# Performance work log

Hardware: AMD Instinct MI355X
Metric: run time of the kernel (lower is better)

The kernel has to match this reference:

```python
import jax, jax.numpy as jnp
import numpy as np

B, P, C = 8, 20000, 64
NX, NY = 432, 496


def setup_inputs() -> dict:
    key = jax.random.key(0)
    k1, k2 = jax.random.split(key)
    pillar_features = jax.random.normal(k1, (B, P, C), dtype=jnp.float32)
    # unique flat cell index per batch so scatter is order-independent
    flat = jax.vmap(lambda k: jax.random.permutation(k, NX * NY)[:P])(
        jax.random.split(k2, B)
    )  # (B, P) int32, unique within each batch
    y = (flat // NX).astype(jnp.int64)
    x = (flat % NX).astype(jnp.int64)
    b = jnp.broadcast_to(jnp.arange(B, dtype=jnp.int64)[:, None], (B, P))
    z = jnp.zeros((B, P), dtype=jnp.int64)
    coords = jnp.stack([b, z, y, x], axis=-1)  # (B, P, 4)
    return {"pillar_features": pillar_features, "coords": coords, "nx": NX, "ny": NY}


def reference(pillar_features, coords, nx, ny):
    # pillar_features: (B, P, C), coords: (B, P, 4) = [batch_idx, z, y, x]
    Bb, Pp, Cc = pillar_features.shape
    idx = coords[:, :, 2] * nx + coords[:, :, 3]          # (B, P) flat y*nx + x
    canvas = jnp.zeros((Bb, ny * nx, Cc), dtype=pillar_features.dtype)
    canvas = canvas.at[jnp.arange(Bb)[:, None], idx].set(pillar_features)
    return canvas.transpose(0, 2, 1).reshape(Bb, Cc, ny, nx)  # (B, C, ny, nx)
```

## Files before the change

### kernel.cpp

```cpp
#include <hip/hip_runtime.h>


#define BB    8
#define PP    20000
#define CC    64
#define NXX   432
#define NYY   496
#define NCELL (NXX * NYY)
#define NCELL4 (NCELL / 4)

#define GBLK   64
#define GNWG   ((BB * NCELL4) / GBLK)
#define NXCD   8
#define CHUNK  (GNWG / NXCD)

typedef float f32x4 __attribute__((ext_vector_type(4)));
typedef unsigned short u16;
typedef u16 u16x4 __attribute__((ext_vector_type(4)));

__global__ void ppsc_scatter_map(const int* __restrict__ coords, u16* __restrict__ map16) {
    int t = blockIdx.x * blockDim.x + threadIdx.x;
    if (t >= BB * PP) return;
    int b = t / PP;
    int p = t - b * PP;
    const int4 c4 = ((const int4*)coords)[t];
    int y = c4.z, x = c4.w;
    if ((unsigned)y < (unsigned)NYY && (unsigned)x < (unsigned)NXX)
        map16[(size_t)b * NCELL + y * NXX + x] = (u16)p;
}

__global__ void __launch_bounds__(GBLK, 8) ppsc_gather_all(const float* __restrict__ pf,
                                                           const u16* __restrict__ map16,
                                                           const int* __restrict__ coords,
                                                           float* __restrict__ out) {
    int bid = blockIdx.x;
    int wg  = (bid % NXCD) * CHUNK + bid / NXCD;

    int t  = wg * GBLK + threadIdx.x;
    int i4 = t % NCELL4;
    int b  = t / NCELL4;

    u16x4 m = ((const u16x4*)(map16 + (size_t)b * NCELL))[i4];
    const int4* cb = ((const int4*)coords) + (size_t)b * PP;
    int cell0 = i4 * 4;

    bool v0 = (m.x < PP), v1 = (m.y < PP), v2 = (m.z < PP), v3 = (m.w < PP);
    if (v0) { int4 c = cb[m.x]; v0 = (c.z * NXX + c.w) == cell0;     }
    if (v1) { int4 c = cb[m.y]; v1 = (c.z * NXX + c.w) == cell0 + 1; }
    if (v2) { int4 c = cb[m.z]; v2 = (c.z * NXX + c.w) == cell0 + 2; }
    if (v3) { int4 c = cb[m.w]; v3 = (c.z * NXX + c.w) == cell0 + 3; }

    const float* base = pf + (size_t)b * PP * CC;
    const float* p0 = base + (size_t)m.x * CC;
    const float* p1 = base + (size_t)m.y * CC;
    const float* p2 = base + (size_t)m.z * CC;
    const float* p3 = base + (size_t)m.w * CC;

    float* ob = out + (size_t)b * CC * NCELL + (size_t)cell0;

#pragma unroll 4
    for (int cq = 0; cq < 16; ++cq) {
        f32x4 o0 = (f32x4)0.f, o1 = (f32x4)0.f, o2 = (f32x4)0.f, o3 = (f32x4)0.f;
        if (v0) { f32x4 f = *(const f32x4*)(p0 + cq * 4);
                  o0.x = f.x; o1.x = f.y; o2.x = f.z; o3.x = f.w; }
        if (v1) { f32x4 f = *(const f32x4*)(p1 + cq * 4);
                  o0.y = f.x; o1.y = f.y; o2.y = f.z; o3.y = f.w; }
        if (v2) { f32x4 f = *(const f32x4*)(p2 + cq * 4);
                  o0.z = f.x; o1.z = f.y; o2.z = f.z; o3.z = f.w; }
        if (v3) { f32x4 f = *(const f32x4*)(p3 + cq * 4);
                  o0.w = f.x; o1.w = f.y; o2.w = f.z; o3.w = f.w; }
        float* op = ob + (size_t)(cq * 4) * NCELL;
        __builtin_nontemporal_store(o0, (f32x4*)op);
        __builtin_nontemporal_store(o1, (f32x4*)(op + (size_t)NCELL));
        __builtin_nontemporal_store(o2, (f32x4*)(op + 2 * (size_t)NCELL));
        __builtin_nontemporal_store(o3, (f32x4*)(op + 3 * (size_t)NCELL));
    }
}

__global__ void ppsc_zero(float* __restrict__ out, int n4) {
    int t = blockIdx.x * blockDim.x + threadIdx.x;
    if (t < n4) ((float4*)out)[t] = make_float4(0.f, 0.f, 0.f, 0.f);
}

__global__ void ppsc_direct_scatter(const float* __restrict__ pf,
                                    const int* __restrict__ coords,
                                    float* __restrict__ out) {
    int t = blockIdx.x * blockDim.x + threadIdx.x;
    if (t >= BB * PP * CC) return;
    int c  = t % CC;
    int bp = t / CC;
    int b  = bp / PP;
    const int* cd = coords + (size_t)bp * 4;
    int y = cd[2], x = cd[3];
    if ((unsigned)y < (unsigned)NYY && (unsigned)x < (unsigned)NXX)
        out[((size_t)(b * CC + c)) * NCELL + (size_t)y * NXX + x] = pf[(size_t)bp * CC + c];
}

extern "C" void kernel_launch(void* const* d_in, const int* in_sizes, int n_in,
                              void* d_out, int out_size, void* d_ws, size_t ws_size,
                              hipStream_t stream) {
    const float* pf     = (const float*)d_in[0];
    const int*   coords = (const int*)d_in[1];
    float*       out    = (float*)d_out;

    const size_t map_bytes = (size_t)BB * NCELL * sizeof(u16);

    if (ws_size >= map_bytes) {
        u16* map16 = (u16*)d_ws;

        int npil = BB * PP;
        ppsc_scatter_map<<<(npil + 255) / 256, 256, 0, stream>>>(coords, map16);

        ppsc_gather_all<<<GNWG, GBLK, 0, stream>>>(pf, map16, coords, out);
    } else {
        int n4_out = out_size / 4;
        ppsc_zero<<<(n4_out + 255) / 256, 256, 0, stream>>>(out, n4_out);

        int nsc = BB * PP * CC;
        ppsc_direct_scatter<<<(nsc + 255) / 256, 256, 0, stream>>>(pf, coords, out);
    }
}
```

Measured before the change: 94.67 us.

## Process two cell groups per thread in gather and XCD-swizzle scatter map

The gather kernel now handles two 4-cell groups per thread (first and second half of the canvas), halving the grid and doubling the loads and stores in flight per thread. The block-to-XCD swizzle is generalized to handle non-divisible grid sizes and is also applied to the scatter-map kernel, which now launches 64-thread blocks. The aim is more memory-level parallelism per wave and better L2 locality per XCD, at the cost of higher register use and possibly lower occupancy.

Result: slower. 130.1 us (+37.4%).

```diff
diff --git a/kernel.cpp b/kernel.cpp
--- a/kernel.cpp
+++ b/kernel.cpp
@@ -8,21 +8,33 @@
 #define NYY   496
 #define NCELL (NXX * NYY)
 #define NCELL4 (NCELL / 4)
+#define HALF4 (NCELL4 / 2)
 
 #define GBLK   64
-#define GNWG   ((BB * NCELL4) / GBLK)
+#define GNWG   ((BB * HALF4) / GBLK)
 #define NXCD   8
-#define CHUNK  (GNWG / NXCD)
+#define SWZ_Q  (GNWG / NXCD)
+#define SWZ_R  (GNWG % NXCD)
+
+#define SNWG   ((BB * PP) / GBLK)
+#define SSWZ_Q (SNWG / NXCD)
+#define SSWZ_R (SNWG % NXCD)
 
 typedef float f32x4 __attribute__((ext_vector_type(4)));
 typedef unsigned short u16;
 typedef u16 u16x4 __attribute__((ext_vector_type(4)));
 
-__global__ void ppsc_scatter_map(const int* __restrict__ coords, u16* __restrict__ map16) {
-    int t = blockIdx.x * blockDim.x + threadIdx.x;
-    if (t >= BB * PP) return;
-    int b = t / PP;
-    int p = t - b * PP;
+__device__ __forceinline__ int xcd_chunk(int bid, int q, int r) {
+    int xcd = bid % NXCD, idx = bid / NXCD;
+    return (xcd < r ? xcd * (q + 1) : r * (q + 1) + (xcd - r) * q) + idx;
+}
+
+__global__ void __launch_bounds__(GBLK) ppsc_scatter_map(const int* __restrict__ coords,
+                                                         u16* __restrict__ map16) {
+    int wg = xcd_chunk(blockIdx.x, SSWZ_Q, SSWZ_R);
+    int t  = wg * GBLK + threadIdx.x;
+    int b  = t / PP;
+    int p  = t - b * PP;
     const int4 c4 = ((const int4*)coords)[t];
     int y = c4.z, x = c4.w;
     if ((unsigned)y < (unsigned)NYY && (unsigned)x < (unsigned)NXX)
@@ -33,47 +45,72 @@
                                                            const u16* __restrict__ map16,
                                                            const int* __restrict__ coords,
                                                            float* __restrict__ out) {
-    int bid = blockIdx.x;
-    int wg  = (bid % NXCD) * CHUNK + bid / NXCD;
+    int wg = xcd_chunk(blockIdx.x, SWZ_Q, SWZ_R);
+    int t  = wg * GBLK + threadIdx.x;
+    int i4 = t % HALF4;
+    int b  = t / HALF4;
 
-    int t  = wg * GBLK + threadIdx.x;
-    int i4 = t % NCELL4;
-    int b  = t / NCELL4;
+    const u16x4* mrow = (const u16x4*)(map16 + (size_t)b * NCELL);
+    u16x4 mA = mrow[i4];
+    u16x4 mB = mrow[i4 + HALF4];
+    const int4* cb = ((const int4*)coords) + (size_t)b * PP;
+    int cellA = i4 * 4;
+    int cellB = (i4 + HALF4) * 4;
 
-    u16x4 m = ((const u16x4*)(map16 + (size_t)b * NCELL))[i4];
-    const int4* cb = ((const int4*)coords) + (size_t)b * PP;
-    int cell0 = i4 * 4;
-
-    bool v0 = (m.x < PP), v1 = (m.y < PP), v2 = (m.z < PP), v3 = (m.w < PP);
-    if (v0) { int4 c = cb[m.x]; v0 = (c.z * NXX + c.w) == cell0;     }
-    if (v1) { int4 c = cb[m.y]; v1 = (c.z * NXX + c.w) == cell0 + 1; }
-    if (v2) { int4 c = cb[m.z]; v2 = (c.z * NXX + c.w) == cell0 + 2; }
-    if (v3) { int4 c = cb[m.w]; v3 = (c.z * NXX + c.w) == cell0 + 3; }
+    bool a0 = (mA.x < PP), a1 = (mA.y < PP), a2 = (mA.z < PP), a3 = (mA.w < PP);
+    bool b0 = (mB.x < PP), b1 = (mB.y < PP), b2 = (mB.z < PP), b3 = (mB.w < PP);
+    if (a0) { int4 c = cb[mA.x]; a0 = (c.z * NXX + c.w) == cellA;     }
+    if (a1) { int4 c = cb[mA.y]; a1 = (c.z * NXX + c.w) == cellA + 1; }
+    if (a2) { int4 c = cb[mA.z]; a2 = (c.z * NXX + c.w) == cellA + 2; }
+    if (a3) { int4 c = cb[mA.w]; a3 = (c.z * NXX + c.w) == cellA + 3; }
+    if (b0) { int4 c = cb[mB.x]; b0 = (c.z * NXX + c.w) == cellB;     }
+    if (b1) { int4 c = cb[mB.y]; b1 = (c.z * NXX + c.w) == cellB + 1; }
+    if (b2) { int4 c = cb[mB.z]; b2 = (c.z * NXX + c.w) == cellB + 2; }
+    if (b3) { int4 c = cb[mB.w]; b3 = (c.z * NXX + c.w) == cellB + 3; }
 
     const float* base = pf + (size_t)b * PP * CC;
-    const float* p0 = base + (size_t)m.x * CC;
-    const float* p1 = base + (size_t)m.y * CC;
-    const float* p2 = base + (size_t)m.z * CC;
-    const float* p3 = base + (size_t)m.w * CC;
+    const float* pa0 = base + (size_t)mA.x * CC;
+    const float* pa1 = base + (size_t)mA.y * CC;
+    const float* pa2 = base + (size_t)mA.z * CC;
+    const float* pa3 = base + (size_t)mA.w * CC;
+    const float* pb0 = base + (size_t)mB.x * CC;
+    const float* pb1 = base + (size_t)mB.y * CC;
+    const float* pb2 = base + (size_t)mB.z * CC;
+    const float* pb3 = base + (size_t)mB.w * CC;
 
-    float* ob = out + (size_t)b * CC * NCELL + (size_t)cell0;
+    float* obA = out + (size_t)b * CC * NCELL + (size_t)cellA;
+    float* obB = out + (size_t)b * CC * NCELL + (size_t)cellB;
 
 #pragma unroll 4
     for (int cq = 0; cq < 16; ++cq) {
-        f32x4 o0 = (f32x4)0.f, o1 = (f32x4)0.f, o2 = (f32x4)0.f, o3 = (f32x4)0.f;
-        if (v0) { f32x4 f = *(const f32x4*)(p0 + cq * 4);
-                  o0.x = f.x; o1.x = f.y; o2.x = f.z; o3.x = f.w; }
-        if (v1) { f32x4 f = *(const f32x4*)(p1 + cq * 4);
-                  o0.y = f.x; o1.y = f.y; o2.y = f.z; o3.y = f.w; }
-        if (v2) { f32x4 f = *(const f32x4*)(p2 + cq * 4);
-                  o0.z = f.x; o1.z = f.y; o2.z = f.z; o3.z = f.w; }
-        if (v3) { f32x4 f = *(const f32x4*)(p3 + cq * 4);
-                  o0.w = f.x; o1.w = f.y; o2.w = f.z; o3.w = f.w; }
-        float* op = ob + (size_t)(cq * 4) * NCELL;
-        __builtin_nontemporal_store(o0, (f32x4*)op);
-        __builtin_nontemporal_store(o1, (f32x4*)(op + (size_t)NCELL));
-        __builtin_nontemporal_store(o2, (f32x4*)(op + 2 * (size_t)NCELL));
-        __builtin_nontemporal_store(o3, (f32x4*)(op + 3 * (size_t)NCELL));
+        f32x4 oA0 = (f32x4)0.f, oA1 = (f32x4)0.f, oA2 = (f32x4)0.f, oA3 = (f32x4)0.f;
+        f32x4 oB0 = (f32x4)0.f, oB1 = (f32x4)0.f, oB2 = (f32x4)0.f, oB3 = (f32x4)0.f;
+        if (a0) { f32x4 f = *(const f32x4*)(pa0 + cq * 4);
+                  oA0.x = f.x; oA1.x = f.y; oA2.x = f.z; oA3.x = f.w; }
+        if (a1) { f32x4 f = *(const f32x4*)(pa1 + cq * 4);
+                  oA0.y = f.x; oA1.y = f.y; oA2.y = f.z; oA3.y = f.w; }
+        if (a2) { f32x4 f = *(const f32x4*)(pa2 + cq * 4);
+                  oA0.z = f.x; oA1.z = f.y; oA2.z = f.z; oA3.z = f.w; }
+        if (a3) { f32x4 f = *(const f32x4*)(pa3 + cq * 4);
+                  oA0.w = f.x; oA1.w = f.y; oA2.w = f.z; oA3.w = f.w; }
+        if (b0) { f32x4 f = *(const f32x4*)(pb0 + cq * 4);
+                  oB0.x = f.x; oB1.x = f.y; oB2.x = f.z; oB3.x = f.w; }
+        if (b1) { f32x4 f = *(const f32x4*)(pb1 + cq * 4);
+                  oB0.y = f.x; oB1.y = f.y; oB2.y = f.z; oB3.y = f.w; }
+        if (b2) { f32x4 f = *(const f32x4*)(pb2 + cq * 4);
+                  oB0.z = f.x; oB1.z = f.y; oB2.z = f.z; oB3.z = f.w; }
+        if (b3) { f32x4 f = *(const f32x4*)(pb3 + cq * 4);
+                  oB0.w = f.x; oB1.w = f.y; oB2.w = f.z; oB3.w = f.w; }
+        float* opA = obA + (size_t)(cq * 4) * NCELL;
+        float* opB = obB + (size_t)(cq * 4) * NCELL;
+        __builtin_nontemporal_store(oA0, (f32x4*)opA);
+        __builtin_nontemporal_store(oA1, (f32x4*)(opA + (size_t)NCELL));
+        __builtin_nontemporal_store(oA2, (f32x4*)(opA + 2 * (size_t)NCELL));
+        __builtin_nontemporal_store(oA3, (f32x4*)(opA + 3 * (size_t)NCELL));
+        __builtin_nontemporal_store(oB0, (f32x4*)opB);
+        __builtin_nontemporal_store(oB1, (f32x4*)(opB + (size_t)NCELL));
+        __builtin_nontemporal_store(oB2, (f32x4*)(opB + 2 * (size_t)NCELL));
+        __builtin_nontemporal_store(oB3, (f32x4*)(opB + 3 * (size_t)NCELL));
     }
 }
 
@@ -108,9 +145,7 @@
     if (ws_size >= map_bytes) {
         u16* map16 = (u16*)d_ws;
 
-        int npil = BB * PP;
-        ppsc_scatter_map<<<(npil + 255) / 256, 256, 0, stream>>>(coords, map16);
-
+        ppsc_scatter_map<<<SNWG, GBLK, 0, stream>>>(coords, map16);
         ppsc_gather_all<<<GNWG, GBLK, 0, stream>>>(pf, map16, coords, out);
     } else {
         int n4_out = out_size / 4;
```
